# Kernel optimization log

Measured on AMD Instinct MI355X. Metric: run time of the kernel, lower is better.

## Reference

```python
import jax, jax.numpy as jnp
import numpy as np

BATCH, LENGTH, FEAT, RANK = 4096, 128, 4, 64
SCALE = 1.0 / np.sqrt(RANK)  # keep 128-step matrix chain numerically stable


def setup_inputs() -> dict:
    key = jax.random.key(0)
    k1, k2, k3, k4 = jax.random.split(key, 4)
    return {
        "input_data": jax.random.normal(k1, (BATCH, LENGTH, FEAT), dtype=jnp.float32),
        "first_core": jax.random.normal(k2, (FEAT, RANK), dtype=jnp.float32) * SCALE,
        "mid_cores": jax.random.normal(k3, (LENGTH - 2, RANK, FEAT, RANK), dtype=jnp.float32) * SCALE,
        "last_core": jax.random.normal(k4, (RANK, FEAT), dtype=jnp.float32) * SCALE,
    }


def reference(input_data, first_core, mid_cores, last_core):
    # input_data: [b, L, f] -> site-major [L, b, f]
    x = jnp.transpose(input_data, (1, 0, 2))
    # Per-site contraction with the physical (feature) index.
    v0 = jnp.einsum("ir,bi->br", first_core, x[0])            # [b, r]
    mid_mats = jnp.einsum("slir,sbi->sblr", mid_cores, x[1:-1])  # [S, b, r, r]
    last_vec = jnp.einsum("li,bi->bl", last_core, x[-1])      # [b, r]

    # Sequential tensor-train chain: v <- v @ M_s for each middle site.
    def step(v, mat):
        return jnp.einsum("bl,blr->br", v, mat), None

    v, _ = jax.lax.scan(step, v0, mid_mats)
    # Final contraction against last site vector -> [b, 1]
    out = jnp.sum(v * last_vec, axis=-1, keepdims=True)
    return out
```

## Files before the change

kernel.cpp:

```cpp
#include <hip/hip_runtime.h>
#include <hip/hip_fp16.h>
#include <stdint.h>

#define NSITES 126
#define XPITCH 516
#define VPITCH 68

typedef _Float16 half8_t  __attribute__((ext_vector_type(8)));
typedef float    float4_t __attribute__((ext_vector_type(4)));

#define LBAR() asm volatile("s_waitcnt lgkmcnt(0)\n\ts_barrier" ::: "memory")
#define WAITV(N) asm volatile("s_waitcnt vmcnt(" #N ")" ::: "memory")
#define TIE8(F) asm volatile("" : "+v"(F[0]), "+v"(F[1]), "+v"(F[2]), "+v"(F[3]), \
                                  "+v"(F[4]), "+v"(F[5]), "+v"(F[6]), "+v"(F[7]))

__device__ __forceinline__ void aload(half8_t& d, const void* p) {
    asm volatile("global_load_dwordx4 %0, %1, off" : "=v"(d) : "v"(p));
}

__global__ __launch_bounds__(256) void repack_g(const float* __restrict__ mid,
                                                _Float16* __restrict__ gt) {
    __shared__ float lds[64 * 260];
    const int s = blockIdx.x;
    const int t = threadIdx.x;
    const float* src = mid + (size_t)s * 16384;
#pragma unroll
    for (int k = 0; k < 16; ++k) {
        const int f4 = t + 256 * k;
        const int l = f4 >> 6, n0 = (f4 & 63) * 4;
        *(float4_t*)&lds[l * 260 + n0] = *(const float4_t*)&src[f4 * 4];
    }
    __syncthreads();
    half8_t* dst = (half8_t*)gt + (size_t)s * 2048;
#pragma unroll
    for (int m = 0; m < 8; ++m) {
        const int F = t + 256 * m;
        const int lane = F & 63, w = (F >> 6) & 3, h = (F >> 8) & 1, i = F >> 9;
        const int q = lane >> 4, c = lane & 15;
        const int n = i * 64 + w * 16 + c;
        half8_t o;
#pragma unroll
        for (int j = 0; j < 8; ++j)
            o[j] = (_Float16)lds[(32 * h + 8 * q + j) * 260 + n];
        dst[F] = o;
    }
}

__global__ __launch_bounds__(256) void tt_chain(
    const float* __restrict__ x,
    const float* __restrict__ first,
    const float* __restrict__ last,
    const _Float16* __restrict__ gt,
    float* __restrict__ out) {

    __shared__ float vbuf[2][16 * VPITCH];
    __shared__ float xbuf[16 * XPITCH];
    __shared__ int   eacc[16];

    const int tid  = threadIdx.x;
    const int w    = tid >> 6;
    const int lane = tid & 63;
    const int q    = lane >> 4;
    const int c    = lane & 15;
    const int b0   = blockIdx.x * 16;

    {
        const int bb = tid >> 4, seg = tid & 15;
        const float4_t* src = (const float4_t*)(x + (size_t)(b0 + bb) * 512 + seg * 32);
        float4_t* dst = (float4_t*)(xbuf + bb * XPITCH + seg * 32);
#pragma unroll
        for (int k = 0; k < 8; ++k) dst[k] = src[k];
    }
    if (tid < 16) eacc[tid] = 0;
    __syncthreads();

    {
        const int bb = tid >> 4, rq = tid & 15;
        const float xs0 = xbuf[bb * XPITCH + 0], xs1 = xbuf[bb * XPITCH + 1];
        const float xs2 = xbuf[bb * XPITCH + 2], xs3 = xbuf[bb * XPITCH + 3];
#pragma unroll
        for (int k = 0; k < 4; ++k) {
            const int r = rq * 4 + k;
            vbuf[0][bb * VPITCH + r] =
                xs0 * first[r] + xs1 * first[64 + r] + xs2 * first[128 + r] + xs3 * first[192 + r];
        }
    }

    half8_t F0[8], F1[8], F2[8];
    const char* gbase = (const char*)gt + w * 1024 + lane * 16;
    auto LOAD = [&](int s, half8_t* F) {
        const char* p = gbase + (size_t)s * 32768;
#pragma unroll
        for (int ih = 0; ih < 8; ++ih) aload(F[ih], p + ih * 4096);
    };
    LOAD(0, F0);
    LOAD(1, F1);
    LBAR();

    auto STEP = [&](int s, half8_t* F) {
        WAITV(16);
        TIE8(F);

        const int p = s & 1;
        const float* vr = &vbuf[p][c * VPITCH];
        float4_t a0lo = *(const float4_t*)(vr + q * 8);
        float4_t a0hi = *(const float4_t*)(vr + q * 8 + 4);
        float4_t a1lo = *(const float4_t*)(vr + 32 + q * 8);
        float4_t a1hi = *(const float4_t*)(vr + 32 + q * 8 + 4);

        if ((s & 7) == 0 && s != 0) {
            float m = 0.f;
#pragma unroll
            for (int k = 0; k < 4; ++k) {
                m = fmaxf(m, fabsf(a0lo[k])); m = fmaxf(m, fabsf(a0hi[k]));
                m = fmaxf(m, fabsf(a1lo[k])); m = fmaxf(m, fabsf(a1hi[k]));
            }
            m = fmaxf(m, __shfl_xor(m, 16));
            m = fmaxf(m, __shfl_xor(m, 32));
            int e = 0;
            if (m > 0.f) frexpf(m, &e);
            const float sc = ldexpf(1.0f, -e);
#pragma unroll
            for (int k = 0; k < 4; ++k) {
                a0lo[k] *= sc; a0hi[k] *= sc; a1lo[k] *= sc; a1hi[k] *= sc;
            }
            if (tid < 16) eacc[tid] += e;
        }

        half8_t af0, af1;
#pragma unroll
        for (int k = 0; k < 4; ++k) {
            af0[k] = (_Float16)a0lo[k]; af0[4 + k] = (_Float16)a0hi[k];
            af1[k] = (_Float16)a1lo[k]; af1[4 + k] = (_Float16)a1hi[k];
        }

        float4_t xs[4];
#pragma unroll
        for (int jj = 0; jj < 4; ++jj)
            xs[jj] = *(const float4_t*)(xbuf + (q * 4 + jj) * XPITCH + (s + 1) * 4);

        float4_t acc[4];
#pragma unroll
        for (int i = 0; i < 4; ++i) {
            float4_t z = {0.f, 0.f, 0.f, 0.f};
            z = __builtin_amdgcn_mfma_f32_16x16x32_f16(af0, F[i * 2 + 0], z, 0, 0, 0);
            z = __builtin_amdgcn_mfma_f32_16x16x32_f16(af1, F[i * 2 + 1], z, 0, 0, 0);
            acc[i] = z;
        }

#pragma unroll
        for (int jj = 0; jj < 4; ++jj) {
            const float vn = xs[jj].x * acc[0][jj] + xs[jj].y * acc[1][jj] +
                             xs[jj].z * acc[2][jj] + xs[jj].w * acc[3][jj];
            vbuf[p ^ 1][(q * 4 + jj) * VPITCH + w * 16 + c] = vn;
        }
        LBAR();
    };

    for (int s = 0; s < NSITES; s += 3) {
        const int s2 = (s + 2 < NSITES) ? s + 2 : NSITES - 1;
        const int s3 = (s + 3 < NSITES) ? s + 3 : NSITES - 1;
        const int s4 = (s + 4 < NSITES) ? s + 4 : NSITES - 1;
        LOAD(s2, F2);
        STEP(s, F0);
        LOAD(s3, F0);
        STEP(s + 1, F1);
        LOAD(s4, F1);
        STEP(s + 2, F2);
    }
    WAITV(0);

    {
        const int bb = tid >> 4, rq = tid & 15;
        const float x0 = xbuf[bb * XPITCH + 508], x1 = xbuf[bb * XPITCH + 509];
        const float x2 = xbuf[bb * XPITCH + 510], x3 = xbuf[bb * XPITCH + 511];
        float dot = 0.f;
#pragma unroll
        for (int k = 0; k < 4; ++k) {
            const int r = rq * 4 + k;
            const float lv = last[r * 4 + 0] * x0 + last[r * 4 + 1] * x1 +
                             last[r * 4 + 2] * x2 + last[r * 4 + 3] * x3;
            dot += lv * vbuf[0][bb * VPITCH + r];
        }
#pragma unroll
        for (int o = 8; o > 0; o >>= 1) dot += __shfl_xor(dot, o, 16);
        if (rq == 0) out[b0 + bb] = ldexpf(dot, eacc[bb]);
    }
}

extern "C" void kernel_launch(void* const* d_in, const int* in_sizes, int n_in,
                              void* d_out, int out_size, void* d_ws, size_t ws_size,
                              hipStream_t stream) {
    (void)in_sizes; (void)n_in; (void)out_size; (void)ws_size;
    const float* x     = (const float*)d_in[0];
    const float* first = (const float*)d_in[1];
    const float* mid   = (const float*)d_in[2];
    const float* last  = (const float*)d_in[3];
    float* out = (float*)d_out;
    _Float16* gt = (_Float16*)d_ws;

    repack_g<<<126, 256, 0, stream>>>(mid, gt);
    tt_chain<<<256, 256, 0, stream>>>(x, first, last, gt, out);
}
```

Measured before the change: 121.4 us.

## Process 32 batch rows per block, store chain vector in fp16, simplify repack

Each block of the chain kernel now handles two 16-row batch groups per site, so every loaded fp16 core slice feeds twice as many MFMAs, and the grid drops to 128 blocks. The inter-step vector buffer is kept in fp16 so the A operand loads straight from LDS without conversion. The input x is staged in two halves to fit LDS, with a mid-loop reload. The repack kernel is rewritten as a direct per-thread strided gather over 1008 blocks with no LDS. Risks: 128 blocks cannot fill all CUs of the device, the serial chain per block gets longer, and the extra fp16 rounding of the running vector may cost accuracy.

```diff
diff --git a/kernel.cpp b/kernel.cpp
--- a/kernel.cpp
+++ b/kernel.cpp
@@ -3,8 +3,8 @@
 #include <stdint.h>
 
 #define NSITES 126
-#define XPITCH 516
-#define VPITCH 68
+#define XP2 260
+#define VPH 72
 
 typedef _Float16 half8_t  __attribute__((ext_vector_type(8)));
 typedef float    float4_t __attribute__((ext_vector_type(4)));
@@ -20,30 +20,15 @@
 
 __global__ __launch_bounds__(256) void repack_g(const float* __restrict__ mid,
                                                 _Float16* __restrict__ gt) {
-    __shared__ float lds[64 * 260];
-    const int s = blockIdx.x;
-    const int t = threadIdx.x;
-    const float* src = mid + (size_t)s * 16384;
-#pragma unroll
-    for (int k = 0; k < 16; ++k) {
-        const int f4 = t + 256 * k;
-        const int l = f4 >> 6, n0 = (f4 & 63) * 4;
-        *(float4_t*)&lds[l * 260 + n0] = *(const float4_t*)&src[f4 * 4];
-    }
-    __syncthreads();
-    half8_t* dst = (half8_t*)gt + (size_t)s * 2048;
-#pragma unroll
-    for (int m = 0; m < 8; ++m) {
-        const int F = t + 256 * m;
-        const int lane = F & 63, w = (F >> 6) & 3, h = (F >> 8) & 1, i = F >> 9;
-        const int q = lane >> 4, c = lane & 15;
-        const int n = i * 64 + w * 16 + c;
-        half8_t o;
-#pragma unroll
-        for (int j = 0; j < 8; ++j)
-            o[j] = (_Float16)lds[(32 * h + 8 * q + j) * 260 + n];
-        dst[F] = o;
-    }
+    const int F = blockIdx.x * 256 + threadIdx.x;
+    const int lane = F & 63, w = (F >> 6) & 3, h = (F >> 8) & 1, i = (F >> 9) & 3;
+    const int s = F >> 11;
+    const int q = lane >> 4, c = lane & 15;
+    const float* src = mid + (size_t)s * 16384 + (32 * h + 8 * q) * 256 + i * 64 + w * 16 + c;
+    half8_t o;
+#pragma unroll
+    for (int j = 0; j < 8; ++j) o[j] = (_Float16)src[j * 256];
+    ((half8_t*)gt)[F] = o;
 }
 
 __global__ __launch_bounds__(256) void tt_chain(
@@ -53,36 +38,40 @@
     const _Float16* __restrict__ gt,
     float* __restrict__ out) {
 
-    __shared__ float vbuf[2][16 * VPITCH];
-    __shared__ float xbuf[16 * XPITCH];
-    __shared__ int   eacc[16];
+    __shared__ __align__(16) _Float16 vbuf[2][2][16 * VPH];
+    __shared__ __align__(16) float    xbuf[32 * XP2];
+    __shared__ int eacc[32];
 
     const int tid  = threadIdx.x;
     const int w    = tid >> 6;
     const int lane = tid & 63;
     const int q    = lane >> 4;
     const int c    = lane & 15;
-    const int b0   = blockIdx.x * 16;
+    const int b0   = blockIdx.x * 32;
 
     {
-        const int bb = tid >> 4, seg = tid & 15;
-        const float4_t* src = (const float4_t*)(x + (size_t)(b0 + bb) * 512 + seg * 32);
-        float4_t* dst = (float4_t*)(xbuf + bb * XPITCH + seg * 32);
-#pragma unroll
-        for (int k = 0; k < 8; ++k) dst[k] = src[k];
-    }
-    if (tid < 16) eacc[tid] = 0;
+        const int bb = tid >> 3, seg = tid & 7;
+        const float4_t* src = (const float4_t*)(x + (size_t)(b0 + bb) * 512) + seg;
+        float4_t* dst = (float4_t*)(xbuf + bb * XP2) + seg;
+#pragma unroll
+        for (int k = 0; k < 8; ++k) dst[k * 8] = src[k * 8];
+    }
+    if (tid < 32) eacc[tid] = 0;
     __syncthreads();
 
     {
         const int bb = tid >> 4, rq = tid & 15;
-        const float xs0 = xbuf[bb * XPITCH + 0], xs1 = xbuf[bb * XPITCH + 1];
-        const float xs2 = xbuf[bb * XPITCH + 2], xs3 = xbuf[bb * XPITCH + 3];
-#pragma unroll
-        for (int k = 0; k < 4; ++k) {
-            const int r = rq * 4 + k;
-            vbuf[0][bb * VPITCH + r] =
-                xs0 * first[r] + xs1 * first[64 + r] + xs2 * first[128 + r] + xs3 * first[192 + r];
+#pragma unroll
+        for (int g = 0; g < 2; ++g) {
+            const int row = g * 16 + bb;
+            const float xs0 = xbuf[row * XP2 + 0], xs1 = xbuf[row * XP2 + 1];
+            const float xs2 = xbuf[row * XP2 + 2], xs3 = xbuf[row * XP2 + 3];
+#pragma unroll
+            for (int k = 0; k < 4; ++k) {
+                const int r = rq * 4 + k;
+                vbuf[g][0][bb * VPH + r] = (_Float16)(xs0 * first[r] + xs1 * first[64 + r] +
+                                                      xs2 * first[128 + r] + xs3 * first[192 + r]);
+            }
         }
     }
 
@@ -97,47 +86,36 @@
     LOAD(1, F1);
     LBAR();
 
-    auto STEP = [&](int s, half8_t* F) {
-        WAITV(16);
-        TIE8(F);
-
-        const int p = s & 1;
-        const float* vr = &vbuf[p][c * VPITCH];
-        float4_t a0lo = *(const float4_t*)(vr + q * 8);
-        float4_t a0hi = *(const float4_t*)(vr + q * 8 + 4);
-        float4_t a1lo = *(const float4_t*)(vr + 32 + q * 8);
-        float4_t a1hi = *(const float4_t*)(vr + 32 + q * 8 + 4);
+    auto GSTEP = [&](int s, int p, half8_t* F, int g) {
+        const _Float16* vr = &vbuf[g][p][c * VPH];
+        half8_t af0 = *(const half8_t*)(vr + q * 8);
+        half8_t af1 = *(const half8_t*)(vr + 32 + q * 8);
 
         if ((s & 7) == 0 && s != 0) {
+            float a[16];
+#pragma unroll
+            for (int k = 0; k < 8; ++k) { a[k] = (float)af0[k]; a[8 + k] = (float)af1[k]; }
             float m = 0.f;
 #pragma unroll
-            for (int k = 0; k < 4; ++k) {
-                m = fmaxf(m, fabsf(a0lo[k])); m = fmaxf(m, fabsf(a0hi[k]));
-                m = fmaxf(m, fabsf(a1lo[k])); m = fmaxf(m, fabsf(a1hi[k]));
-            }
+            for (int k = 0; k < 16; ++k) m = fmaxf(m, fabsf(a[k]));
             m = fmaxf(m, __shfl_xor(m, 16));
             m = fmaxf(m, __shfl_xor(m, 32));
             int e = 0;
             if (m > 0.f) frexpf(m, &e);
             const float sc = ldexpf(1.0f, -e);
 #pragma unroll
-            for (int k = 0; k < 4; ++k) {
-                a0lo[k] *= sc; a0hi[k] *= sc; a1lo[k] *= sc; a1hi[k] *= sc;
+            for (int k = 0; k < 8; ++k) {
+                af0[k] = (_Float16)(a[k] * sc);
+                af1[k] = (_Float16)(a[8 + k] * sc);
             }
-            if (tid < 16) eacc[tid] += e;
-        }
-
-        half8_t af0, af1;
-#pragma unroll
-        for (int k = 0; k < 4; ++k) {
-            af0[k] = (_Float16)a0lo[k]; af0[4 + k] = (_Float16)a0hi[k];
-            af1[k] = (_Float16)a1lo[k]; af1[4 + k] = (_Float16)a1hi[k];
-        }
-
+            if (tid < 16) eacc[g * 16 + tid] += e;
+        }
+
+        const int xcol = ((s + 1) * 4) & 255;
         float4_t xs[4];
 #pragma unroll
         for (int jj = 0; jj < 4; ++jj)
-            xs[jj] = *(const float4_t*)(xbuf + (q * 4 + jj) * XPITCH + (s + 1) * 4);
+            xs[jj] = *(const float4_t*)(xbuf + (g * 16 + q * 4 + jj) * XP2 + xcol);
 
         float4_t acc[4];
 #pragma unroll
@@ -147,13 +125,21 @@
             z = __builtin_amdgcn_mfma_f32_16x16x32_f16(af1, F[i * 2 + 1], z, 0, 0, 0);
             acc[i] = z;
         }
-
+        _Float16* wr = &vbuf[g][p ^ 1][0];
 #pragma unroll
         for (int jj = 0; jj < 4; ++jj) {
             const float vn = xs[jj].x * acc[0][jj] + xs[jj].y * acc[1][jj] +
                              xs[jj].z * acc[2][jj] + xs[jj].w * acc[3][jj];
-            vbuf[p ^ 1][(q * 4 + jj) * VPITCH + w * 16 + c] = vn;
-        }
+            wr[(q * 4 + jj) * VPH + w * 16 + c] = (_Float16)vn;
+        }
+    };
+
+    auto SITE = [&](int s, half8_t* F) {
+        WAITV(16);
+        TIE8(F);
+        const int p = s & 1;
+        GSTEP(s, p, F, 0);
+        GSTEP(s, p, F, 1);
         LBAR();
     };
 
@@ -162,29 +148,41 @@
         const int s3 = (s + 3 < NSITES) ? s + 3 : NSITES - 1;
         const int s4 = (s + 4 < NSITES) ? s + 4 : NSITES - 1;
         LOAD(s2, F2);
-        STEP(s, F0);
+        SITE(s, F0);
         LOAD(s3, F0);
-        STEP(s + 1, F1);
+        SITE(s + 1, F1);
         LOAD(s4, F1);
-        STEP(s + 2, F2);
+        SITE(s + 2, F2);
+        if (s == 60) {
+            const int bb = tid >> 3, seg = tid & 7;
+            const float4_t* src = (const float4_t*)(x + (size_t)(b0 + bb) * 512 + 256) + seg;
+            float4_t* dst = (float4_t*)(xbuf + bb * XP2) + seg;
+#pragma unroll
+            for (int k = 0; k < 8; ++k) dst[k * 8] = src[k * 8];
+            LBAR();
+        }
     }
     WAITV(0);
 
     {
         const int bb = tid >> 4, rq = tid & 15;
-        const float x0 = xbuf[bb * XPITCH + 508], x1 = xbuf[bb * XPITCH + 509];
-        const float x2 = xbuf[bb * XPITCH + 510], x3 = xbuf[bb * XPITCH + 511];
-        float dot = 0.f;
-#pragma unroll
-        for (int k = 0; k < 4; ++k) {
-            const int r = rq * 4 + k;
-            const float lv = last[r * 4 + 0] * x0 + last[r * 4 + 1] * x1 +
-                             last[r * 4 + 2] * x2 + last[r * 4 + 3] * x3;
-            dot += lv * vbuf[0][bb * VPITCH + r];
-        }
-#pragma unroll
-        for (int o = 8; o > 0; o >>= 1) dot += __shfl_xor(dot, o, 16);
-        if (rq == 0) out[b0 + bb] = ldexpf(dot, eacc[bb]);
+#pragma unroll
+        for (int g = 0; g < 2; ++g) {
+            const int row = g * 16 + bb;
+            const float x0 = xbuf[row * XP2 + 252], x1 = xbuf[row * XP2 + 253];
+            const float x2 = xbuf[row * XP2 + 254], x3 = xbuf[row * XP2 + 255];
+            float dot = 0.f;
+#pragma unroll
+            for (int k = 0; k < 4; ++k) {
+                const int r = rq * 4 + k;
+                const float lv = last[r * 4 + 0] * x0 + last[r * 4 + 1] * x1 +
+                                 last[r * 4 + 2] * x2 + last[r * 4 + 3] * x3;
+                dot += lv * (float)vbuf[g][0][bb * VPH + r];
+            }
+#pragma unroll
+            for (int o = 8; o > 0; o >>= 1) dot += __shfl_xor(dot, o, 16);
+            if (rq == 0) out[b0 + row] = ldexpf(dot, eacc[g * 16 + bb]);
+        }
     }
 }
 
@@ -199,6 +197,6 @@
     float* out = (float*)d_out;
     _Float16* gt = (_Float16*)d_ws;
 
-    repack_g<<<126, 256, 0, stream>>>(mid, gt);
-    tt_chain<<<256, 256, 0, stream>>>(x, first, last, gt, out);
-}
+    repack_g<<<1008, 256, 0, stream>>>(mid, gt);
+    tt_chain<<<128, 256, 0, stream>>>(x, first, last, gt, out);
+}
```

Result: slower. 151.1 us (+24.5%).

## Store chain vector in fp16 LDS, hoist loads, and simplify repack kernel

Applied to the files above, without the earlier changes.

The state vector buffer in shared memory now holds fp16 instead of fp32, so each step reads two 16-byte vectors directly as MFMA operands with no conversion, and writes back half-precision values. The LDS reads of the vector and x values are moved ahead of the global-load wait so they can overlap with outstanding weight loads. The repack kernel drops its shared-memory transpose and has each thread gather its 8 strided floats directly, launched over more blocks. Rounding the intermediate vector to fp16 at every step adds precision loss along the 126-step chain, and the strided gathers in repack may coalesce less well.

```diff
diff --git a/kernel.cpp b/kernel.cpp
--- a/kernel.cpp
+++ b/kernel.cpp
@@ -1,10 +1,9 @@
 #include <hip/hip_runtime.h>
-#include <hip/hip_fp16.h>
 #include <stdint.h>
 
 #define NSITES 126
 #define XPITCH 516
-#define VPITCH 68
+#define VPH    72
 
 typedef _Float16 half8_t  __attribute__((ext_vector_type(8)));
 typedef float    float4_t __attribute__((ext_vector_type(4)));
@@ -20,30 +19,15 @@
 
 __global__ __launch_bounds__(256) void repack_g(const float* __restrict__ mid,
                                                 _Float16* __restrict__ gt) {
-    __shared__ float lds[64 * 260];
-    const int s = blockIdx.x;
-    const int t = threadIdx.x;
-    const float* src = mid + (size_t)s * 16384;
+    const int F = blockIdx.x * 256 + threadIdx.x;
+    const int lane = F & 63, w = (F >> 6) & 3, h = (F >> 8) & 1, i = (F >> 9) & 3;
+    const int s = F >> 11;
+    const int q = lane >> 4, c = lane & 15;
+    const float* src = mid + (size_t)s * 16384 + (32 * h + 8 * q) * 256 + i * 64 + w * 16 + c;
+    half8_t o;
 #pragma unroll
-    for (int k = 0; k < 16; ++k) {
-        const int f4 = t + 256 * k;
-        const int l = f4 >> 6, n0 = (f4 & 63) * 4;
-        *(float4_t*)&lds[l * 260 + n0] = *(const float4_t*)&src[f4 * 4];
-    }
-    __syncthreads();
-    half8_t* dst = (half8_t*)gt + (size_t)s * 2048;
-#pragma unroll
-    for (int m = 0; m < 8; ++m) {
-        const int F = t + 256 * m;
-        const int lane = F & 63, w = (F >> 6) & 3, h = (F >> 8) & 1, i = F >> 9;
-        const int q = lane >> 4, c = lane & 15;
-        const int n = i * 64 + w * 16 + c;
-        half8_t o;
-#pragma unroll
-        for (int j = 0; j < 8; ++j)
-            o[j] = (_Float16)lds[(32 * h + 8 * q + j) * 260 + n];
-        dst[F] = o;
-    }
+    for (int j = 0; j < 8; ++j) o[j] = (_Float16)src[j * 256];
+    ((half8_t*)gt)[F] = o;
 }
 
 __global__ __launch_bounds__(256) void tt_chain(
@@ -53,7 +37,7 @@
     const _Float16* __restrict__ gt,
     float* __restrict__ out) {
 
-    __shared__ float vbuf[2][16 * VPITCH];
+    __shared__ __align__(16) _Float16 vbuf[2][16 * VPH];
     __shared__ float xbuf[16 * XPITCH];
     __shared__ int   eacc[16];
 
@@ -81,8 +65,8 @@
 #pragma unroll
         for (int k = 0; k < 4; ++k) {
             const int r = rq * 4 + k;
-            vbuf[0][bb * VPITCH + r] =
-                xs0 * first[r] + xs1 * first[64 + r] + xs2 * first[128 + r] + xs3 * first[192 + r];
+            vbuf[0][bb * VPH + r] = (_Float16)(
+                xs0 * first[r] + xs1 * first[64 + r] + xs2 * first[128 + r] + xs3 * first[192 + r]);
         }
     }
 
@@ -98,46 +82,38 @@
     LBAR();
 
     auto STEP = [&](int s, half8_t* F) {
+        const int p = s & 1;
+
+        const _Float16* vr = &vbuf[p][c * VPH];
+        half8_t af0 = *(const half8_t*)(vr + q * 8);
+        half8_t af1 = *(const half8_t*)(vr + 32 + q * 8);
+        float4_t xs[4];
+#pragma unroll
+        for (int jj = 0; jj < 4; ++jj)
+            xs[jj] = *(const float4_t*)(xbuf + (q * 4 + jj) * XPITCH + (s + 1) * 4);
+
         WAITV(16);
         TIE8(F);
 
-        const int p = s & 1;
-        const float* vr = &vbuf[p][c * VPITCH];
-        float4_t a0lo = *(const float4_t*)(vr + q * 8);
-        float4_t a0hi = *(const float4_t*)(vr + q * 8 + 4);
-        float4_t a1lo = *(const float4_t*)(vr + 32 + q * 8);
-        float4_t a1hi = *(const float4_t*)(vr + 32 + q * 8 + 4);
-
         if ((s & 7) == 0 && s != 0) {
+            float a[16];
+#pragma unroll
+            for (int k = 0; k < 8; ++k) { a[k] = (float)af0[k]; a[8 + k] = (float)af1[k]; }
             float m = 0.f;
 #pragma unroll
-            for (int k = 0; k < 4; ++k) {
-                m = fmaxf(m, fabsf(a0lo[k])); m = fmaxf(m, fabsf(a0hi[k]));
-                m = fmaxf(m, fabsf(a1lo[k])); m = fmaxf(m, fabsf(a1hi[k]));
-            }
+            for (int k = 0; k < 16; ++k) m = fmaxf(m, fabsf(a[k]));
             m = fmaxf(m, __shfl_xor(m, 16));
             m = fmaxf(m, __shfl_xor(m, 32));
             int e = 0;
             if (m > 0.f) frexpf(m, &e);
             const float sc = ldexpf(1.0f, -e);
 #pragma unroll
-            for (int k = 0; k < 4; ++k) {
-                a0lo[k] *= sc; a0hi[k] *= sc; a1lo[k] *= sc; a1hi[k] *= sc;
+            for (int k = 0; k < 8; ++k) {
+                af0[k] = (_Float16)(a[k] * sc);
+                af1[k] = (_Float16)(a[8 + k] * sc);
             }
             if (tid < 16) eacc[tid] += e;
         }
-
-        half8_t af0, af1;
-#pragma unroll
-        for (int k = 0; k < 4; ++k) {
-            af0[k] = (_Float16)a0lo[k]; af0[4 + k] = (_Float16)a0hi[k];
-            af1[k] = (_Float16)a1lo[k]; af1[4 + k] = (_Float16)a1hi[k];
-        }
-
-        float4_t xs[4];
-#pragma unroll
-        for (int jj = 0; jj < 4; ++jj)
-            xs[jj] = *(const float4_t*)(xbuf + (q * 4 + jj) * XPITCH + (s + 1) * 4);
 
         float4_t acc[4];
 #pragma unroll
@@ -152,7 +128,7 @@
         for (int jj = 0; jj < 4; ++jj) {
             const float vn = xs[jj].x * acc[0][jj] + xs[jj].y * acc[1][jj] +
                              xs[jj].z * acc[2][jj] + xs[jj].w * acc[3][jj];
-            vbuf[p ^ 1][(q * 4 + jj) * VPITCH + w * 16 + c] = vn;
+            vbuf[p ^ 1][(q * 4 + jj) * VPH + w * 16 + c] = (_Float16)vn;
         }
         LBAR();
     };
@@ -180,7 +156,7 @@
             const int r = rq * 4 + k;
             const float lv = last[r * 4 + 0] * x0 + last[r * 4 + 1] * x1 +
                              last[r * 4 + 2] * x2 + last[r * 4 + 3] * x3;
-            dot += lv * vbuf[0][bb * VPITCH + r];
+            dot += lv * (float)vbuf[0][bb * VPH + r];
         }
 #pragma unroll
         for (int o = 8; o > 0; o >>= 1) dot += __shfl_xor(dot, o, 16);
@@ -199,6 +175,6 @@
     float* out = (float*)d_out;
     _Float16* gt = (_Float16*)d_ws;
 
-    repack_g<<<126, 256, 0, stream>>>(mid, gt);
+    repack_g<<<1008, 256, 0, stream>>>(mid, gt);
     tt_chain<<<256, 256, 0, stream>>>(x, first, last, gt, out);
 }
```

New measurement: 120.8 us. Within noise of the previous version (-0.5%).
